# Performance work log

Hardware: AMD Instinct MI355X
Metric: run time of the kernel (lower is better)

Reference implementation:

```python
import jax, jax.numpy as jnp
import numpy as np

N, L, D_MODEL, N_HEADS = 2, 2048, 512, 8

def setup_inputs() -> dict:
    key = jax.random.key(0)
    x = jax.random.normal(key, (N, L, D_MODEL), dtype=jnp.float32)
    return {"input_data": x}

def reference(input_data):
    n, l, _ = input_data.shape
    h = N_HEADS
    d = D_MODEL // h  # head dim
    # Q = K = V = reshaped input (the Linear projections are unused in the original forward)
    q = input_data.reshape(n, l, h, d)
    k = q
    v = q
    scale = 1.0 / jnp.sqrt(jnp.float32(d))
    # scores: [n, h, l, s]
    scores = jnp.einsum('nlhd,nshd->nhls', q, k)
    attn_weights = jax.nn.softmax(scale * scores, axis=-1)
    # updated values: [n, l, h, d]
    updated_v = jnp.einsum('nhls,nshd->nlhd', attn_weights, v)
    out = updated_v.reshape(n, l, h * d)
    # attn returned as mean over heads: permute nhls -> nlhs, mean over h -> [n, l, s]
    attn = jnp.transpose(attn_weights, (0, 2, 1, 3)).mean(axis=-2)
    return (out, attn)
```

## Files before the change

kernel.cpp:

```cpp
#include <hip/hip_runtime.h>

#define NBATCH 2
#define SEQ    2048
#define DMODEL 512
#define NH     8
#define HDIM   64
#define SCALE  0.125f

#define K2 0.1803368801111204f

#if __has_builtin(__builtin_amdgcn_exp2f)
#define EXP2(x) __builtin_amdgcn_exp2f(x)
#else
#define EXP2(x) __expf((x) * 0.6931471805599453f)
#endif

typedef __attribute__((ext_vector_type(8))) short bf16x8;
typedef __attribute__((ext_vector_type(4))) float f32x4;

__device__ __forceinline__ unsigned short f2bf(float f) {
    union { float f; unsigned u; } v; v.f = f;
    unsigned r = v.u + 0x7FFFu + ((v.u >> 16) & 1u);
    return (unsigned short)(r >> 16);
}

__device__ __forceinline__ void pack4(unsigned short* dst, float4 v) {
    unsigned long long pk = (unsigned long long)f2bf(v.x)
        | ((unsigned long long)f2bf(v.y) << 16)
        | ((unsigned long long)f2bf(v.z) << 32)
        | ((unsigned long long)f2bf(v.w) << 48);
    __builtin_memcpy(dst, &pk, 8);
}

__device__ __forceinline__ bf16x8 pack8(float4 a, float4 b) {
    bf16x8 r;
    r[0]=(short)f2bf(a.x); r[1]=(short)f2bf(a.y); r[2]=(short)f2bf(a.z); r[3]=(short)f2bf(a.w);
    r[4]=(short)f2bf(b.x); r[5]=(short)f2bf(b.y); r[6]=(short)f2bf(b.z); r[7]=(short)f2bf(b.w);
    return r;
}

__device__ __forceinline__ void gld_lds16(const unsigned short* g, unsigned short* l) {
    __builtin_amdgcn_global_load_lds(
        (const __attribute__((address_space(1))) unsigned int*)(const void*)g,
        (__attribute__((address_space(3))) unsigned int*)(void*)l, 16, 0, 0);
}

__global__ __launch_bounds__(256) void prep_kernel(const float* __restrict__ x,
                                                   unsigned short* __restrict__ xb,
                                                   unsigned short* __restrict__ xt) {
    __shared__ unsigned short Tb[64][72];
    const int bid = blockIdx.x;
    const int n = bid >> 8, h = (bid >> 5) & 7, st = bid & 31;
    const int s0 = st * 64;
    const int t = threadIdx.x;
    {
        const int s = t >> 2, d0 = (t & 3) * 16;
        const float* xp = x + ((size_t)(n*SEQ + s0 + s))*DMODEL + h*HDIM + d0;
        #pragma unroll
        for (int i = 0; i < 4; ++i) pack4(&Tb[s][d0 + 4*i], *(const float4*)(xp + 4*i));
    }
    __syncthreads();
    {
        const int s = t >> 2, d0 = (t & 3) * 16;
        unsigned short* bp = xb + ((size_t)(n*SEQ + s0 + s))*DMODEL + h*HDIM + d0;
        *(bf16x8*)bp       = *(const bf16x8*)&Tb[s][d0];
        *(bf16x8*)(bp + 8) = *(const bf16x8*)&Tb[s][d0 + 8];
    }
    {
        const int d = t >> 2, c0 = (t & 3) * 16;
        bf16x8 v0, v1;
        #pragma unroll
        for (int j = 0; j < 8; ++j) {
            v0[j] = (short)Tb[c0 + j][d];
            v1[j] = (short)Tb[c0 + 8 + j][d];
        }
        unsigned short* tp = xt + ((size_t)((n*NH + h)*HDIM + d))*SEQ + s0 + c0;
        *(bf16x8*)tp       = v0;
        *(bf16x8*)(tp + 8) = v1;
    }
}

__global__ __launch_bounds__(256) void out_kernel4(const unsigned short* __restrict__ xb,
                                                   const unsigned short* __restrict__ xt,
                                                   float* __restrict__ out,
                                                   float* __restrict__ rho) {
    __shared__ unsigned short Kb[2][64*64];
    __shared__ unsigned short Vt[2][64*64];
    __shared__ unsigned short pb[64][72];

    const int i   = blockIdx.x;
    const int bid = (i & 7) * 64 + (i >> 3);
    const int n = bid >> 8, h = (bid >> 5) & 7, lt = bid & 31;
    const int l0 = lt * 64;
    const int tid = threadIdx.x;
    const int wv = tid >> 6, lane = tid & 63;
    const int lr = lane & 15, lg = lane >> 4;

    const unsigned short* qp = xb + ((size_t)(n*SEQ + l0 + wv*16 + lr))*DMODEL + h*HDIM + lg*8;
    const bf16x8 a0 = *(const bf16x8*)qp;
    const bf16x8 a1 = *(const bf16x8*)(qp + 32);

    bf16x8 ones;
    #pragma unroll
    for (int j = 0; j < 8; ++j) ones[j] = (short)0x3F80;

    const int srow8  = wv*8 + (lane >> 3);
    const int schunk = lane & 7;
    const unsigned short* kbase = xb + (size_t)(n*SEQ)*DMODEL + h*HDIM;
    const unsigned short* vbase = xt + ((size_t)(n*NH + h)*HDIM)*SEQ;

    auto stage = [&](int buf, int s0) {
        #pragma unroll
        for (int it = 0; it < 2; ++it) {
            const int row = it*32 + srow8;
            const int gc  = schunk ^ (row & 7);
            gld_lds16(kbase + (size_t)(s0 + row)*DMODEL + gc*8,
                      &Kb[buf][it*2048 + wv*512]);
        }
        #pragma unroll
        for (int it = 0; it < 2; ++it) {
            const int d  = it*32 + srow8;
            const int gc = schunk ^ (d & 7);
            gld_lds16(vbase + (size_t)d*SEQ + s0 + gc*8,
                      &Vt[buf][it*2048 + wv*512]);
        }
    };

    f32x4 ov0 = {0.f,0.f,0.f,0.f}, ov1 = {0.f,0.f,0.f,0.f};
    f32x4 ov2 = {0.f,0.f,0.f,0.f}, ov3 = {0.f,0.f,0.f,0.f};
    f32x4 ovS = {0.f,0.f,0.f,0.f};

    stage(0, 0);
    __syncthreads();
    int cur = 0;

    for (int c = 0; c < 32; ++c) {
        if (c < 31) stage(cur ^ 1, (c + 1) * 64);

        const int c0 = (lg ^ (lr & 7)) << 3;
        #pragma unroll
        for (int ct = 0; ct < 4; ++ct) {
            const unsigned short* kr = &Kb[cur][(ct*16 + lr)*64];
            bf16x8 b0 = *(const bf16x8*)&kr[c0];
            bf16x8 b1 = *(const bf16x8*)&kr[c0 ^ 32];
            f32x4 acc = {0.f,0.f,0.f,0.f};
            acc = __builtin_amdgcn_mfma_f32_16x16x32_bf16(b0, a0, acc, 0,0,0);
            acc = __builtin_amdgcn_mfma_f32_16x16x32_bf16(b1, a1, acc, 0,0,0);
            const float e0 = EXP2(acc[0] * K2);
            const float e1 = EXP2(acc[1] * K2);
            const float e2 = EXP2(acc[2] * K2);
            const float e3 = EXP2(acc[3] * K2);
            unsigned long long pk = (unsigned long long)f2bf(e0)
                | ((unsigned long long)f2bf(e1) << 16)
                | ((unsigned long long)f2bf(e2) << 32)
                | ((unsigned long long)f2bf(e3) << 48);
            __builtin_memcpy(&pb[wv*16 + lr][ct*16 + lg*4], &pk, 8);
        }
        #pragma unroll
        for (int ks = 0; ks < 2; ++ks) {
            const bf16x8 pa = *(const bf16x8*)&pb[wv*16 + lr][ks*32 + lg*8];
            const int cc = ((ks*4 + lg) ^ (lr & 7)) << 3;
            const bf16x8 w0 = *(const bf16x8*)&Vt[cur][( 0 + lr)*64 + cc];
            const bf16x8 w1 = *(const bf16x8*)&Vt[cur][(16 + lr)*64 + cc];
            const bf16x8 w2 = *(const bf16x8*)&Vt[cur][(32 + lr)*64 + cc];
            const bf16x8 w3 = *(const bf16x8*)&Vt[cur][(48 + lr)*64 + cc];
            ov0 = __builtin_amdgcn_mfma_f32_16x16x32_bf16(pa, w0, ov0, 0,0,0);
            ov1 = __builtin_amdgcn_mfma_f32_16x16x32_bf16(pa, w1, ov1, 0,0,0);
            ov2 = __builtin_amdgcn_mfma_f32_16x16x32_bf16(pa, w2, ov2, 0,0,0);
            ov3 = __builtin_amdgcn_mfma_f32_16x16x32_bf16(pa, w3, ov3, 0,0,0);
            ovS = __builtin_amdgcn_mfma_f32_16x16x32_bf16(pa, ones, ovS, 0,0,0);
        }
        __syncthreads();
        cur ^= 1;
    }

    const int row0 = l0 + wv*16 + lg*4;
    if (lr == 0) {
        #pragma unroll
        for (int r = 0; r < 4; ++r)
            rho[(size_t)(n*NH + h)*SEQ + row0 + r] = ovS[r];
    }
    #pragma unroll
    for (int r = 0; r < 4; ++r) {
        const float iv = 1.f / ovS[r];
        float* op = out + ((size_t)(n*SEQ + row0 + r))*DMODEL + h*HDIM + lr;
        op[0]  = ov0[r] * iv;
        op[16] = ov1[r] * iv;
        op[32] = ov2[r] * iv;
        op[48] = ov3[r] * iv;
    }
}

__global__ __launch_bounds__(256) void mean_kernel4(const unsigned short* __restrict__ xb,
                                                    const float* __restrict__ rho,
                                                    float* __restrict__ attn) {
    __shared__ unsigned short Qb[2][64*64];
    __shared__ unsigned short Kb[2][64*64];
    __shared__ float invb[NH][64];

    const int i   = blockIdx.x;
    const int bid = (i & 7) * 256 + (i >> 3);
    const int n = bid >> 10, lt = (bid >> 5) & 31, st = bid & 31;
    const int l0 = lt * 64, s0 = st * 64;
    const int tid = threadIdx.x;
    const int wv = tid >> 6, lane = tid & 63;
    const int lr = lane & 15, lg = lane >> 4;

    for (int j = tid; j < NH*64; j += 256) {
        const int hh = j >> 6, row = j & 63;
        invb[hh][row] = 0.125f / rho[(size_t)(n*NH + hh)*SEQ + l0 + row];
    }

    const int srow8  = wv*8 + (lane >> 3);
    const int schunk = lane & 7;

    auto stage = [&](int buf, int h) {
        #pragma unroll
        for (int it = 0; it < 2; ++it) {
            const int row = it*32 + srow8;
            const int gc  = schunk ^ (row & 7);
            gld_lds16(xb + ((size_t)(n*SEQ + l0 + row))*DMODEL + h*HDIM + gc*8,
                      &Qb[buf][it*2048 + wv*512]);
        }
        #pragma unroll
        for (int it = 0; it < 2; ++it) {
            const int row = it*32 + srow8;
            const int gc  = schunk ^ (row & 7);
            gld_lds16(xb + ((size_t)(n*SEQ + s0 + row))*DMODEL + h*HDIM + gc*8,
                      &Kb[buf][it*2048 + wv*512]);
        }
    };

    float mean[4][4];
    #pragma unroll
    for (int ct = 0; ct < 4; ++ct)
        #pragma unroll
        for (int r = 0; r < 4; ++r) mean[ct][r] = 0.f;

    stage(0, 0);
    __syncthreads();
    int cur = 0;

    for (int h = 0; h < NH; ++h) {
        if (h < NH-1) stage(cur ^ 1, h + 1);

        const int qrow = wv*16 + lr;
        const int c0 = (lg ^ (lr & 7)) << 3;
        const bf16x8 a0 = *(const bf16x8*)&Qb[cur][qrow*64 + c0];
        const bf16x8 a1 = *(const bf16x8*)&Qb[cur][qrow*64 + (c0 ^ 32)];
        const float logiv = __log2f(invb[h][wv*16 + lr]);
        #pragma unroll
        for (int ct = 0; ct < 4; ++ct) {
            const unsigned short* kr = &Kb[cur][(ct*16 + lr)*64];
            bf16x8 b0 = *(const bf16x8*)&kr[c0];
            bf16x8 b1 = *(const bf16x8*)&kr[c0 ^ 32];
            f32x4 acc = {0.f,0.f,0.f,0.f};
            acc = __builtin_amdgcn_mfma_f32_16x16x32_bf16(b0, a0, acc, 0,0,0);
            acc = __builtin_amdgcn_mfma_f32_16x16x32_bf16(b1, a1, acc, 0,0,0);
            #pragma unroll
            for (int r = 0; r < 4; ++r)
                mean[ct][r] += EXP2(fmaf(acc[r], K2, logiv));
        }
        __syncthreads();
        cur ^= 1;
    }

    const int arow = n*SEQ + l0 + wv*16 + lr;
    #pragma unroll
    for (int ct = 0; ct < 4; ++ct) {
        float4 v = { mean[ct][0], mean[ct][1], mean[ct][2], mean[ct][3] };
        *(float4*)&attn[(size_t)arow*SEQ + s0 + ct*16 + lg*4] = v;
    }
}

__global__ __launch_bounds__(256) void fb_out_kernel(const float* __restrict__ x,
                                                     float* __restrict__ out,
                                                     float* __restrict__ rho) {
    __shared__ unsigned short Kbuf[128][72];
    __shared__ unsigned short vT[64][136];
    __shared__ unsigned short pbuf[64][136];
    const int bid = blockIdx.x;
    const int n  = bid >> 8, h = (bid >> 5) & 7, lt = bid & 31;
    const int l0 = lt * 64;
    const int tid = threadIdx.x;
    const int wv  = tid >> 6, lane = tid & 63;
    const int lr  = lane & 15, lg = lane >> 4;
    const float* qp = x + ((size_t)(n*SEQ + l0 + wv*16 + lr))*DMODEL + h*HDIM + lg*8;
    const bf16x8 a0 = pack8(*(const float4*)qp,      *(const float4*)(qp+4));
    const bf16x8 a1 = pack8(*(const float4*)(qp+32), *(const float4*)(qp+36));
    f32x4 ov0 = {0.f,0.f,0.f,0.f}, ov1 = {0.f,0.f,0.f,0.f};
    f32x4 ov2 = {0.f,0.f,0.f,0.f}, ov3 = {0.f,0.f,0.f,0.f};
    float rs[4] = {0.f,0.f,0.f,0.f};
    for (int s0 = 0; s0 < SEQ; s0 += 128) {
        __syncthreads();
        {
            const int srow = tid >> 1, dbase = (tid & 1) * 32;
            const float* kp = x + ((size_t)(n*SEQ + s0 + srow))*DMODEL + h*HDIM + dbase;
            #pragma unroll
            for (int i = 0; i < 8; ++i) {
                float4 v = *(const float4*)(kp + 4*i);
                pack4(&Kbuf[srow][dbase + 4*i], v);
                const int d = dbase + 4*i;
                vT[d+0][srow] = f2bf(v.x); vT[d+1][srow] = f2bf(v.y);
                vT[d+2][srow] = f2bf(v.z); vT[d+3][srow] = f2bf(v.w);
            }
        }
        __syncthreads();
        #pragma unroll
        for (int ct = 0; ct < 8; ++ct) {
            const unsigned short* bp = &Kbuf[ct*16 + lr][lg*8];
            bf16x8 b0 = *(const bf16x8*)bp;
            bf16x8 b1 = *(const bf16x8*)(bp + 32);
            f32x4 acc = {0.f,0.f,0.f,0.f};
            acc = __builtin_amdgcn_mfma_f32_16x16x32_bf16(a0, b0, acc, 0,0,0);
            acc = __builtin_amdgcn_mfma_f32_16x16x32_bf16(a1, b1, acc, 0,0,0);
            #pragma unroll
            for (int r = 0; r < 4; ++r) {
                const float e = __expf(acc[r] * SCALE);
                rs[r] += e;
                pbuf[wv*16 + lg*4 + r][ct*16 + lr] = f2bf(e);
            }
        }
        __syncthreads();
        #pragma unroll
        for (int ks = 0; ks < 4; ++ks) {
            bf16x8 pa = *(const bf16x8*)&pbuf[wv*16 + lr][ks*32 + lg*8];
            bf16x8 v0 = *(const bf16x8*)&vT[ 0 + lr][ks*32 + lg*8];
            bf16x8 v1 = *(const bf16x8*)&vT[16 + lr][ks*32 + lg*8];
            bf16x8 v2 = *(const bf16x8*)&vT[32 + lr][ks*32 + lg*8];
            bf16x8 v3 = *(const bf16x8*)&vT[48 + lr][ks*32 + lg*8];
            ov0 = __builtin_amdgcn_mfma_f32_16x16x32_bf16(pa, v0, ov0, 0,0,0);
            ov1 = __builtin_amdgcn_mfma_f32_16x16x32_bf16(pa, v1, ov1, 0,0,0);
            ov2 = __builtin_amdgcn_mfma_f32_16x16x32_bf16(pa, v2, ov2, 0,0,0);
            ov3 = __builtin_amdgcn_mfma_f32_16x16x32_bf16(pa, v3, ov3, 0,0,0);
        }
    }
    #pragma unroll
    for (int r = 0; r < 4; ++r) {
        float s = rs[r];
        s += __shfl_xor(s, 1, 16); s += __shfl_xor(s, 2, 16);
        s += __shfl_xor(s, 4, 16); s += __shfl_xor(s, 8, 16);
        rs[r] = s;
    }
    const int row0 = l0 + wv*16 + lg*4;
    if (lr == 0) {
        #pragma unroll
        for (int r = 0; r < 4; ++r)
            rho[(size_t)(n*NH + h)*SEQ + row0 + r] = rs[r];
    }
    #pragma unroll
    for (int r = 0; r < 4; ++r) {
        const float iv = 1.f / rs[r];
        float* op = out + ((size_t)(n*SEQ + row0 + r))*DMODEL + h*HDIM + lr;
        op[0] = ov0[r]*iv; op[16] = ov1[r]*iv; op[32] = ov2[r]*iv; op[48] = ov3[r]*iv;
    }
}

__global__ __launch_bounds__(256) void fb_mean_kernel(const float* __restrict__ x,
                                                      const float* __restrict__ rho,
                                                      float* __restrict__ attn) {
    __shared__ unsigned short Qb[64][72];
    __shared__ unsigned short Kb[128][72];
    __shared__ float          invb[64];
    const int bid = blockIdx.x;
    const int n  = bid >> 9, lt = (bid >> 4) & 31, st = bid & 15;
    const int l0 = lt * 64, s0 = st * 128;
    const int tid = threadIdx.x;
    const int wv  = tid >> 6, lane = tid & 63;
    const int lr  = lane & 15, lg = lane >> 4;
    float mean[8][4];
    #pragma unroll
    for (int ct = 0; ct < 8; ++ct)
        #pragma unroll
        for (int r = 0; r < 4; ++r) mean[ct][r] = 0.f;
    for (int h = 0; h < NH; ++h) {
        __syncthreads();
        {
            const int qrow = tid >> 2, qd = (tid & 3) * 16;
            const float* qp = x + ((size_t)(n*SEQ + l0 + qrow))*DMODEL + h*HDIM + qd;
            #pragma unroll
            for (int i = 0; i < 4; ++i)
                pack4(&Qb[qrow][qd + 4*i], *(const float4*)(qp + 4*i));
        }
        {
            const int srow = tid >> 1, dbase = (tid & 1) * 32;
            const float* kp = x + ((size_t)(n*SEQ + s0 + srow))*DMODEL + h*HDIM + dbase;
            #pragma unroll
            for (int i = 0; i < 8; ++i)
                pack4(&Kb[srow][dbase + 4*i], *(const float4*)(kp + 4*i));
        }
        if (tid < 64)
            invb[tid] = 0.125f / rho[(size_t)(n*NH + h)*SEQ + l0 + tid];
        __syncthreads();
        const unsigned short* ap = &Qb[wv*16 + lr][lg*8];
        const bf16x8 a0 = *(const bf16x8*)ap;
        const bf16x8 a1 = *(const bf16x8*)(ap + 32);
        #pragma unroll
        for (int ct = 0; ct < 8; ++ct) {
            const unsigned short* bp = &Kb[ct*16 + lr][lg*8];
            bf16x8 b0 = *(const bf16x8*)bp;
            bf16x8 b1 = *(const bf16x8*)(bp + 32);
            f32x4 acc = {0.f,0.f,0.f,0.f};
            acc = __builtin_amdgcn_mfma_f32_16x16x32_bf16(a0, b0, acc, 0,0,0);
            acc = __builtin_amdgcn_mfma_f32_16x16x32_bf16(a1, b1, acc, 0,0,0);
            #pragma unroll
            for (int r = 0; r < 4; ++r)
                mean[ct][r] += __expf(acc[r] * SCALE) * invb[wv*16 + lg*4 + r];
        }
    }
    #pragma unroll
    for (int ct = 0; ct < 8; ++ct)
        #pragma unroll
        for (int r = 0; r < 4; ++r)
            attn[((size_t)(n*SEQ + l0 + wv*16 + lg*4 + r))*SEQ + s0 + ct*16 + lr]
                = mean[ct][r];
}

extern "C" void kernel_launch(void* const* d_in, const int* in_sizes, int n_in,
                              void* d_out, int out_size, void* d_ws, size_t ws_size,
                              hipStream_t stream) {
    (void)in_sizes; (void)n_in; (void)out_size;
    const float* x = (const float*)d_in[0];
    float* out  = (float*)d_out;
    float* attn = out + (size_t)NBATCH*SEQ*DMODEL;
    float* rho  = (float*)d_ws;

    const size_t XB_OFF = 131072;
    const size_t XT_OFF = XB_OFF + 4194304;
    const size_t NEED   = XT_OFF + 4194304;

    if (ws_size >= NEED) {
        unsigned short* xb = (unsigned short*)((char*)d_ws + XB_OFF);
        unsigned short* xt = (unsigned short*)((char*)d_ws + XT_OFF);
        prep_kernel <<<dim3(512),  dim3(256), 0, stream>>>(x, xb, xt);
        out_kernel4 <<<dim3(512),  dim3(256), 0, stream>>>(xb, xt, out, rho);
        mean_kernel4<<<dim3(2048), dim3(256), 0, stream>>>(xb, rho, attn);
    } else {
        fb_out_kernel <<<dim3(512),  dim3(256), 0, stream>>>(x, out, rho);
        fb_mean_kernel<<<dim3(1024), dim3(256), 0, stream>>>(x, rho, attn);
    }
}
```

Before: 81.68 us.

## Split out_kernel key range in two and add combine kernel

Splits the attention-output kernel's key loop into two halves processed by separate blocks, doubling the grid from 512 to 1024 blocks to fill more compute units. Each block writes unnormalized partial outputs and row sums to a workspace buffer, and a new combine kernel sums the two halves, normalizes, and writes out and rho. This works because no max subtraction is used, so the partials can be summed directly. It adds an extra kernel launch and about 17 MB of partial-buffer traffic, and it only takes effect when the workspace is large enough.

```diff
diff --git a/kernel.cpp b/kernel.cpp
--- a/kernel.cpp
+++ b/kernel.cpp
@@ -83,15 +83,23 @@
 __global__ __launch_bounds__(256) void out_kernel4(const unsigned short* __restrict__ xb,
                                                    const unsigned short* __restrict__ xt,
                                                    float* __restrict__ out,
-                                                   float* __restrict__ rho) {
+                                                   float* __restrict__ rho,
+                                                   float* __restrict__ part,
+                                                   int split) {
     __shared__ unsigned short Kb[2][64*64];
     __shared__ unsigned short Vt[2][64*64];
     __shared__ unsigned short pb[64][72];
 
     const int i   = blockIdx.x;
-    const int bid = (i & 7) * 64 + (i >> 3);
-    const int n = bid >> 8, h = (bid >> 5) & 7, lt = bid & 31;
+    const int cps = gridDim.x >> 3;
+    const int bid = (i & 7) * cps + (i >> 3);
+    int n, h, lt, ss;
+    if (split) { n = bid >> 9; h = (bid >> 6) & 7; lt = (bid >> 1) & 31; ss = bid & 1; }
+    else       { n = bid >> 8; h = (bid >> 5) & 7; lt = bid & 31;        ss = 0;       }
     const int l0 = lt * 64;
+    const int sbase = ss << 10;
+    const int nch = split ? 16 : 32;
+
     const int tid = threadIdx.x;
     const int wv = tid >> 6, lane = tid & 63;
     const int lr = lane & 15, lg = lane >> 4;
@@ -130,12 +138,12 @@
     f32x4 ov2 = {0.f,0.f,0.f,0.f}, ov3 = {0.f,0.f,0.f,0.f};
     f32x4 ovS = {0.f,0.f,0.f,0.f};
 
-    stage(0, 0);
+    stage(0, sbase);
     __syncthreads();
     int cur = 0;
 
-    for (int c = 0; c < 32; ++c) {
-        if (c < 31) stage(cur ^ 1, (c + 1) * 64);
+    for (int c = 0; c < nch; ++c) {
+        if (c < nch - 1) stage(cur ^ 1, sbase + (c + 1) * 64);
 
         const int c0 = (lg ^ (lr & 7)) << 3;
         #pragma unroll
@@ -174,20 +182,64 @@
         cur ^= 1;
     }
 
-    const int row0 = l0 + wv*16 + lg*4;
-    if (lr == 0) {
-        #pragma unroll
-        for (int r = 0; r < 4; ++r)
-            rho[(size_t)(n*NH + h)*SEQ + row0 + r] = ovS[r];
-    }
-    #pragma unroll
-    for (int r = 0; r < 4; ++r) {
-        const float iv = 1.f / ovS[r];
-        float* op = out + ((size_t)(n*SEQ + row0 + r))*DMODEL + h*HDIM + lr;
-        op[0]  = ov0[r] * iv;
-        op[16] = ov1[r] * iv;
-        op[32] = ov2[r] * iv;
-        op[48] = ov3[r] * iv;
+    if (split) {
+        float* pp = part + ((size_t)(((n*NH + h)*32 + lt)*2 + ss))*4160;
+        #pragma unroll
+        for (int r = 0; r < 4; ++r) {
+            const int qloc = wv*16 + lg*4 + r;
+            float* op = pp + qloc*64 + lr;
+            op[0]  = ov0[r];
+            op[16] = ov1[r];
+            op[32] = ov2[r];
+            op[48] = ov3[r];
+        }
+        if (lr == 0) {
+            #pragma unroll
+            for (int r = 0; r < 4; ++r)
+                pp[4096 + wv*16 + lg*4 + r] = ovS[r];
+        }
+    } else {
+        const int row0 = l0 + wv*16 + lg*4;
+        if (lr == 0) {
+            #pragma unroll
+            for (int r = 0; r < 4; ++r)
+                rho[(size_t)(n*NH + h)*SEQ + row0 + r] = ovS[r];
+        }
+        #pragma unroll
+        for (int r = 0; r < 4; ++r) {
+            const float iv = 1.f / ovS[r];
+            float* op = out + ((size_t)(n*SEQ + row0 + r))*DMODEL + h*HDIM + lr;
+            op[0]  = ov0[r] * iv;
+            op[16] = ov1[r] * iv;
+            op[32] = ov2[r] * iv;
+            op[48] = ov3[r] * iv;
+        }
+    }
+}
+
+__global__ __launch_bounds__(256) void combine_kernel(const float* __restrict__ part,
+                                                      float* __restrict__ out,
+                                                      float* __restrict__ rho) {
+    const int bid = blockIdx.x;
+    const int n = bid >> 8, h = (bid >> 5) & 7, lt = bid & 31;
+    const int l0 = lt * 64;
+    const int tid = threadIdx.x;
+    const int q = tid >> 2, dg = (tid & 3) * 16;
+
+    const float* p0 = part + ((size_t)(((n*NH + h)*32 + lt)*2))*4160;
+    const float* p1 = p0 + 4160;
+    const float rs = p0[4096 + q] + p1[4096 + q];
+    const float iv = 1.f / rs;
+    if ((tid & 3) == 0)
+        rho[(size_t)(n*NH + h)*SEQ + l0 + q] = rs;
+
+    float* op = out + ((size_t)(n*SEQ + l0 + q))*DMODEL + h*HDIM + dg;
+    #pragma unroll
+    for (int i = 0; i < 4; ++i) {
+        float4 a = *(const float4*)&p0[q*64 + dg + 4*i];
+        float4 b = *(const float4*)&p1[q*64 + dg + 4*i];
+        float4 o = { (a.x+b.x)*iv, (a.y+b.y)*iv, (a.z+b.z)*iv, (a.w+b.w)*iv };
+        *(float4*)&op[4*i] = o;
     }
 }
 
@@ -425,15 +477,23 @@
     float* attn = out + (size_t)NBATCH*SEQ*DMODEL;
     float* rho  = (float*)d_ws;
 
-    const size_t XB_OFF = 131072;
-    const size_t XT_OFF = XB_OFF + 4194304;
-    const size_t NEED   = XT_OFF + 4194304;
-
-    if (ws_size >= NEED) {
+    const size_t XB_OFF   = 131072;
+    const size_t XT_OFF   = XB_OFF + 4194304;
+    const size_t NEED1    = XT_OFF + 4194304;
+    const size_t PART_OFF = NEED1;
+    const size_t NEED2    = PART_OFF + (size_t)1024*4160*4;
+
+    if (ws_size >= NEED1) {
         unsigned short* xb = (unsigned short*)((char*)d_ws + XB_OFF);
         unsigned short* xt = (unsigned short*)((char*)d_ws + XT_OFF);
         prep_kernel <<<dim3(512),  dim3(256), 0, stream>>>(x, xb, xt);
-        out_kernel4 <<<dim3(512),  dim3(256), 0, stream>>>(xb, xt, out, rho);
+        if (ws_size >= NEED2) {
+            float* part = (float*)((char*)d_ws + PART_OFF);
+            out_kernel4   <<<dim3(1024), dim3(256), 0, stream>>>(xb, xt, out, rho, part, 1);
+            combine_kernel<<<dim3(512),  dim3(256), 0, stream>>>(part, out, rho);
+        } else {
+            out_kernel4   <<<dim3(512),  dim3(256), 0, stream>>>(xb, xt, out, rho, nullptr, 0);
+        }
         mean_kernel4<<<dim3(2048), dim3(256), 0, stream>>>(xb, rho, attn);
     } else {
         fb_out_kernel <<<dim3(512),  dim3(256), 0, stream>>>(x, out, rho);
```

Measured after the change: 84.69 us. 1.04x slower.
